# Kernel tuning notes

Measured on AMD Instinct MI355X. Metric: run time of the kernel, lower is better.

## Reference

```python
import jax, jax.numpy as jnp
import numpy as np

N_NODES = 100000


def gcn_conv(x, src, dst, W, b, n):
    # PyG GCNConv: x' = D^-1/2 (A + I) D^-1/2 (x W) + b
    h = x @ W  # [N, out] transform first (cheaper when out < in)
    loop = jnp.arange(n, dtype=src.dtype)
    s = jnp.concatenate([src, loop])
    d = jnp.concatenate([dst, loop])
    deg = jax.ops.segment_sum(jnp.ones_like(s, dtype=h.dtype), d, num_segments=n)
    dinv = jnp.where(deg > 0, jax.lax.rsqrt(deg), 0.0)
    norm = dinv[s] * dinv[d]  # [E+N]
    msg = h[s] * norm[:, None]  # [E+N, out]
    agg = jax.ops.segment_sum(msg, d, num_segments=n)
    return agg + b


def setup_inputs() -> dict:
    key = jax.random.key(0)
    ks = jax.random.split(key, 12)
    n, E, labels = N_NODES, 1600000, 128
    edges = jax.random.randint(ks[0], (2, E), 0, n, dtype=jnp.int64)
    features = jax.random.normal(ks[1], (n, labels), dtype=jnp.float32)

    def kaiming(k, fan_in, shape):
        return jax.random.normal(k, shape, dtype=jnp.float32) * np.sqrt(2.0 / fan_in)

    return {
        "edges": edges,
        "features": features,
        "W1": kaiming(ks[2], labels, (labels, 64)),
        "b1": jnp.zeros((64,), jnp.float32),
        "W2": kaiming(ks[3], 64, (64, 32)),
        "b2": jnp.zeros((32,), jnp.float32),
        "W3": kaiming(ks[4], 32, (32, 16)),
        "b3": jnp.zeros((16,), jnp.float32),
        "Wfc": kaiming(ks[5], 112, (112, 16)),
        "bfc": jnp.zeros((16,), jnp.float32),
    }


def reference(edges, features, W1, b1, W2, b2, W3, b3, Wfc, bfc):
    n = features.shape[0]
    src, dst = edges[0], edges[1]
    # eval mode: dropout is identity
    f1 = jax.nn.relu(gcn_conv(features, src, dst, W1, b1, n))  # [N, 64]
    f2 = jax.nn.relu(gcn_conv(f1, src, dst, W2, b2, n))        # [N, 32]
    f3 = jax.nn.relu(gcn_conv(f2, src, dst, W3, b3, n))        # [N, 16]
    cat = jnp.concatenate([f1, f2, f3], axis=1)                 # [N, 112]
    return jax.nn.relu(cat @ Wfc + bfc)                         # [N, 16]
```

## Files before the change

kernel.cpp:

```cpp
#include <hip/hip_runtime.h>

typedef unsigned short u16;
typedef float f32x4 __attribute__((ext_vector_type(4)));
typedef short bf16x8 __attribute__((ext_vector_type(8)));

constexpr int SH = 9;
constexpr int NB = 1 << SH;
constexpr int TILE = 4096;

__device__ inline float bf2f(u16 u) {
  union { unsigned int i; float f; } c;
  c.i = ((unsigned int)u) << 16;
  return c.f;
}
__device__ inline u16 f2bf(float f) {
  union { float f; unsigned int i; } c;
  c.f = f;
  unsigned int r = c.i + 0x7fff + ((c.i >> 16) & 1);
  return (u16)(r >> 16);
}

union V8 {
  bf16x8 v;
  short s[8];
  u16 u[8];
  int i[4];
};


__global__ void __launch_bounds__(256) k_hist(const int* __restrict__ dst,
                                              int* __restrict__ ghist, int E,
                                              int nblk, int nbk) {
  __shared__ int lcnt[NB];
  int t = threadIdx.x, blk = blockIdx.x;
  for (int i = t; i < nbk; i += 256) lcnt[i] = 0;
  __syncthreads();
  int beg = blk * TILE, end = min(beg + TILE, E);
  for (int e = beg + t; e < end; e += 256) atomicAdd(&lcnt[dst[e] >> SH], 1);
  __syncthreads();
  for (int i = t; i < nbk; i += 256) ghist[i * nblk + blk] = lcnt[i];
}

__global__ void __launch_bounds__(256) k_scanA(int* __restrict__ ghist,
                                               int* __restrict__ bsum, int nblk) {
  __shared__ int sc[256];
  int i = blockIdx.x, t = threadIdx.x;
  int* row = ghist + (size_t)i * nblk;
  int e0 = 2 * t, e1 = 2 * t + 1;
  int a0 = (e0 < nblk) ? row[e0] : 0;
  int a1 = (e1 < nblk) ? row[e1] : 0;
  int s = a0 + a1;
  sc[t] = s;
  __syncthreads();
  for (int o = 1; o < 256; o <<= 1) {
    int x = (t >= o) ? sc[t - o] : 0;
    __syncthreads();
    sc[t] += x;
    __syncthreads();
  }
  int base = sc[t] - s;
  if (e0 < nblk) row[e0] = base;
  if (e1 < nblk) row[e1] = base + a0;
  if (t == 255) bsum[i] = sc[255];
}

__global__ void __launch_bounds__(256) k_part(const int* __restrict__ src,
                                              const int* __restrict__ dst,
                                              const int* __restrict__ goff,
                                              const int* __restrict__ bsum,
                                              int* __restrict__ ebuf, int E,
                                              int nblk, int nbk) {
  __shared__ int lcur[NB];
  __shared__ int sb[256];
  int t = threadIdx.x, blk = blockIdx.x;
  int v = (t < nbk) ? bsum[t] : 0;
  sb[t] = v;
  __syncthreads();
  for (int o = 1; o < 256; o <<= 1) {
    int x = (t >= o) ? sb[t - o] : 0;
    __syncthreads();
    sb[t] += x;
    __syncthreads();
  }
  for (int i = t; i < nbk; i += 256)
    lcur[i] = goff[(size_t)i * nblk + blk] + (i ? sb[i - 1] : 0);
  __syncthreads();
  int beg = blk * TILE, end = min(beg + TILE, E);
  for (int e = beg + t; e < end; e += 256) {
    int s = src[e], d = dst[e];
    int p = atomicAdd(&lcur[d >> SH], 1);
    ebuf[p] = s | ((d & (NB - 1)) << 20);
  }
}

__global__ void __launch_bounds__(256) k_refine(
    const int* __restrict__ ebuf, const int* __restrict__ goff,
    const int* __restrict__ bsum, int* __restrict__ rowptr,
    int* __restrict__ colsrc, float* __restrict__ dinv,
    int n, int nbk, int nblk, int E) {
  __shared__ int cnt[NB];
  __shared__ int cur[NB];
  __shared__ int sc[256];
  __shared__ int bex[256];
  int b = blockIdx.x, t = threadIdx.x;
  {
    int v = (t < nbk) ? bsum[t] : 0;
    bex[t] = v;
    __syncthreads();
    for (int o = 1; o < 256; o <<= 1) {
      int x = (t >= o) ? bex[t - o] : 0;
      __syncthreads();
      bex[t] += x;
      __syncthreads();
    }
  }
  int beg = goff[(size_t)b * nblk] + (b ? bex[b - 1] : 0);
  int end = (b + 1 < nbk) ? goff[(size_t)(b + 1) * nblk] + bex[b] : E;
  cnt[t] = 0;
  cnt[t + 256] = 0;
  __syncthreads();
  for (int i = beg + t; i < end; i += 256) atomicAdd(&cnt[ebuf[i] >> 20], 1);
  __syncthreads();
  int c0 = cnt[2 * t], c1 = cnt[2 * t + 1];
  int a = c0 + c1;
  sc[t] = a;
  __syncthreads();
  for (int o = 1; o < 256; o <<= 1) {
    int x = (t >= o) ? sc[t - o] : 0;
    __syncthreads();
    sc[t] += x;
    __syncthreads();
  }
  int base0 = beg + sc[t] - a;
  int base1 = base0 + c0;
  int node0 = b << SH;
  int n0 = node0 + 2 * t, n1 = n0 + 1;
  cur[2 * t] = base0;
  cur[2 * t + 1] = base1;
  if (n0 <= n) rowptr[n0] = base0;
  if (n1 <= n) rowptr[n1] = base1;
  if (n0 < n) dinv[n0] = rsqrtf((float)(c0 + 1));
  if (n1 < n) dinv[n1] = rsqrtf((float)(c1 + 1));
  if (b == nbk - 1 && t == 0) rowptr[n] = E;
  __syncthreads();
  for (int i = beg + t; i < end; i += 256) {
    int w = ebuf[i];
    int p = atomicAdd(&cur[w >> 20], 1);
    colsrc[p] = w & 0xFFFFF;
  }
}


template <int KC, int FOUT, bool BF16IN, int FCROW0, int FCROWS, int MODE>
__global__ void __launch_bounds__(256) k_xform(
    const void* __restrict__ xin, const float* __restrict__ Wg,
    const float* __restrict__ dinv, u16* __restrict__ g,
    const float* __restrict__ Wfc, float* __restrict__ out, int n) {
  constexpr int FIN = KC * 32;
  constexpr int NC = FOUT / 16;
  constexpr int ASLOTS = 8 * KC * 64;
  constexpr int WSLOTS = KC * NC * 64;
  constexpr int WFS = (FCROWS > 0) ? KC * 64 : 1;
  __shared__ short xa[ASLOTS * 8];
  __shared__ short wb[WSLOTS * 8];
  __shared__ short wfb[WFS * 8];

  int t = threadIdx.x;
  int r0 = blockIdx.x * 128;

  for (int s = t; s < WSLOTS; s += 256) {
    int lane = s & 63, q = s >> 6;
    int nc = q % NC, kc = q / NC;
    int col = nc * 16 + (lane & 15);
    int kr = kc * 32 + (lane >> 4) * 8;
    V8 v;
#pragma unroll
    for (int j = 0; j < 8; ++j) v.s[j] = (short)f2bf(Wg[(kr + j) * FOUT + col]);
    *(bf16x8*)&wb[s * 8] = v.v;
  }
  if constexpr (FCROWS > 0) {
    for (int s = t; s < WFS; s += 256) {
      int lane = s & 63, kc = s >> 6;
      int col = lane & 15;
      int kr = kc * 32 + (lane >> 4) * 8;
      V8 v;
#pragma unroll
      for (int j = 0; j < 8; ++j)
        v.s[j] = (kr + j < FCROWS) ? (short)f2bf(Wfc[(FCROW0 + kr + j) * 16 + col]) : (short)0;
      *(bf16x8*)&wfb[s * 8] = v.v;
    }
  }

  for (int s = t; s < ASLOTS; s += 256) {
    int lane = s & 63, q = s >> 6;
    int kc = q % KC, mtile = q / KC;
    int row = mtile * 16 + (lane & 15);
    int k = kc * 32 + (lane >> 4) * 8;
    int gr = r0 + row;
    V8 v;
    if (gr < n) {
      if constexpr (BF16IN) {
        v.v = *(const bf16x8*)((const u16*)xin + (size_t)gr * FIN + k);
      } else {
        const float* xf = (const float*)xin + (size_t)gr * FIN + k;
        float4 p = *(const float4*)xf;
        float4 q4 = *(const float4*)(xf + 4);
        v.s[0] = (short)f2bf(p.x); v.s[1] = (short)f2bf(p.y);
        v.s[2] = (short)f2bf(p.z); v.s[3] = (short)f2bf(p.w);
        v.s[4] = (short)f2bf(q4.x); v.s[5] = (short)f2bf(q4.y);
        v.s[6] = (short)f2bf(q4.z); v.s[7] = (short)f2bf(q4.w);
      }
    } else {
      for (int j = 0; j < 8; ++j) v.s[j] = 0;
    }
    *(bf16x8*)&xa[s * 8] = v.v;
  }
  __syncthreads();

  int ln = t & 63, wv = t >> 6;
  int m0 = wv * 2;

  bf16x8 bf[KC * NC];
#pragma unroll
  for (int i = 0; i < KC * NC; ++i) bf[i] = *(const bf16x8*)&wb[(i * 64 + ln) * 8];
  bf16x8 wff[(FCROWS > 0) ? KC : 1];
  if constexpr (FCROWS > 0) {
#pragma unroll
    for (int i = 0; i < KC; ++i) wff[i] = *(const bf16x8*)&wfb[(i * 64 + ln) * 8];
  }

  f32x4 acc[2][NC];
  f32x4 accF[2];
#pragma unroll
  for (int i = 0; i < 2; ++i) {
    accF[i] = {0.f, 0.f, 0.f, 0.f};
#pragma unroll
    for (int j = 0; j < NC; ++j) acc[i][j] = {0.f, 0.f, 0.f, 0.f};
  }

#pragma unroll
  for (int kc = 0; kc < KC; ++kc) {
    bf16x8 a0 = *(const bf16x8*)&xa[(((m0 + 0) * KC + kc) * 64 + ln) * 8];
    bf16x8 a1 = *(const bf16x8*)&xa[(((m0 + 1) * KC + kc) * 64 + ln) * 8];
#pragma unroll
    for (int nc = 0; nc < NC; ++nc) {
      acc[0][nc] = __builtin_amdgcn_mfma_f32_16x16x32_bf16(a0, bf[kc * NC + nc], acc[0][nc], 0, 0, 0);
      acc[1][nc] = __builtin_amdgcn_mfma_f32_16x16x32_bf16(a1, bf[kc * NC + nc], acc[1][nc], 0, 0, 0);
    }
    if constexpr (FCROWS > 0) {
      accF[0] = __builtin_amdgcn_mfma_f32_16x16x32_bf16(a0, wff[kc], accF[0], 0, 0, 0);
      accF[1] = __builtin_amdgcn_mfma_f32_16x16x32_bf16(a1, wff[kc], accF[1], 0, 0, 0);
    }
  }

  int colb = ln & 15, rq = ln >> 4;
#pragma unroll
  for (int mt2 = 0; mt2 < 2; ++mt2) {
#pragma unroll
    for (int reg = 0; reg < 4; ++reg) {
      int gr = r0 + (m0 + mt2) * 16 + rq * 4 + reg;
      if (gr < n) {
        float di = dinv[gr];
#pragma unroll
        for (int nc = 0; nc < NC; ++nc)
          g[(size_t)gr * FOUT + nc * 16 + colb] = f2bf(acc[mt2][nc][reg] * di);
        if constexpr (FCROWS > 0) {
          size_t oi = (size_t)gr * 16 + colb;
          if constexpr (MODE == 0) out[oi] = accF[mt2][reg];
          else out[oi] += accF[mt2][reg];
        }
      }
    }
  }
}


template <int F>
__global__ void __launch_bounds__(256) k_gather_fin(
    const u16* __restrict__ g, const int* __restrict__ rowptr,
    const int* __restrict__ colsrc, const float* __restrict__ dinv,
    const float* __restrict__ bias, u16* __restrict__ fout, int n) {
  constexpr int LPG = F / 8;
  constexpr int G = 64 / LPG;
  int t = threadIdx.x;
  int ln = t & 63, wib = t >> 6;
  int lanein = ln % LPG, grp = ln / LPG;
  int f0 = lanein * 8;
  float bb[8];
#pragma unroll
  for (int j = 0; j < 8; ++j) bb[j] = bias[f0 + j];
  int gw = blockIdx.x * (blockDim.x >> 6) + wib;
  int nwaves = (gridDim.x * blockDim.x) >> 6;
  for (int node = gw * G + grp; node < n; node += nwaves * G) {
    int b = rowptr[node], e = rowptr[node + 1];
    float p0[8], p1[8], p2[8], p3[8];
    {
      V8 u;
      u.v = *(const bf16x8*)&g[(size_t)node * F + f0];
#pragma unroll
      for (int j = 0; j < 8; ++j) {
        p0[j] = bf2f(u.u[j]);
        p1[j] = 0.f; p2[j] = 0.f; p3[j] = 0.f;
      }
    }
    int i = b;
    for (; i + 4 <= e; i += 4) {
      int s0 = colsrc[i + 0], s1 = colsrc[i + 1];
      int s2 = colsrc[i + 2], s3 = colsrc[i + 3];
      V8 u0, u1, u2, u3;
      u0.v = *(const bf16x8*)&g[(size_t)s0 * F + f0];
      u1.v = *(const bf16x8*)&g[(size_t)s1 * F + f0];
      u2.v = *(const bf16x8*)&g[(size_t)s2 * F + f0];
      u3.v = *(const bf16x8*)&g[(size_t)s3 * F + f0];
#pragma unroll
      for (int j = 0; j < 8; ++j) {
        p0[j] += bf2f(u0.u[j]);
        p1[j] += bf2f(u1.u[j]);
        p2[j] += bf2f(u2.u[j]);
        p3[j] += bf2f(u3.u[j]);
      }
    }
    for (; i < e; ++i) {
      int s = colsrc[i];
      V8 u;
      u.v = *(const bf16x8*)&g[(size_t)s * F + f0];
#pragma unroll
      for (int j = 0; j < 8; ++j) p1[j] += bf2f(u.u[j]);
    }
    float di = dinv[node];
    V8 o;
#pragma unroll
    for (int j = 0; j < 8; ++j) {
      float a = (p0[j] + p1[j]) + (p2[j] + p3[j]);
      o.u[j] = f2bf(fmaxf(fmaf(a, di, bb[j]), 0.f));
    }
    *(bf16x8*)&fout[(size_t)node * F + f0] = o.v;
  }
}


__global__ void __launch_bounds__(256) k_gather_fc(
    const u16* __restrict__ g3, const int* __restrict__ rowptr,
    const int* __restrict__ colsrc, const float* __restrict__ dinv,
    const float* __restrict__ b3, const float* __restrict__ Wfc,
    const float* __restrict__ bfc, float* __restrict__ out, int n) {
  __shared__ short wfb[64 * 8];
  int t = threadIdx.x;
  for (int s = t; s < 64; s += 256) {
    int lane = s & 63;
    int col = lane & 15;
    int kr = (lane >> 4) * 8;
    V8 v;
#pragma unroll
    for (int j = 0; j < 8; ++j)
      v.s[j] = (kr + j < 16) ? (short)f2bf(Wfc[(96 + kr + j) * 16 + col]) : (short)0;
    *(bf16x8*)&wfb[s * 8] = v.v;
  }
  __syncthreads();

  int ln = t & 63, wv = t >> 6;
  bf16x8 wff = *(const bf16x8*)&wfb[ln * 8];
  int lanein = ln & 1, grp = ln >> 1;
  int f0 = lanein * 8;
  float bb[8];
#pragma unroll
  for (int j = 0; j < 8; ++j) bb[j] = b3[f0 + j];
  int colb = ln & 15, rq = ln >> 4, kq = ln >> 4;
  float bfcc = bfc[colb];

  int wid = blockIdx.x * 4 + wv;
  int nw = gridDim.x * 4;
  int nch = (n + 31) / 32;

  for (int ch = wid; ch < nch; ch += nw) {
    int gr = ch * 32 + grp;
    V8 o;
    if (gr < n) {
      int b = rowptr[gr], e = rowptr[gr + 1];
      float p0[8], p1[8], p2[8], p3[8];
      {
        V8 u;
        u.v = *(const bf16x8*)&g3[(size_t)gr * 16 + f0];
#pragma unroll
        for (int j = 0; j < 8; ++j) {
          p0[j] = bf2f(u.u[j]);
          p1[j] = 0.f; p2[j] = 0.f; p3[j] = 0.f;
        }
      }
      int i = b;
      for (; i + 4 <= e; i += 4) {
        int s0 = colsrc[i + 0], s1 = colsrc[i + 1];
        int s2 = colsrc[i + 2], s3 = colsrc[i + 3];
        V8 u0, u1, u2, u3;
        u0.v = *(const bf16x8*)&g3[(size_t)s0 * 16 + f0];
        u1.v = *(const bf16x8*)&g3[(size_t)s1 * 16 + f0];
        u2.v = *(const bf16x8*)&g3[(size_t)s2 * 16 + f0];
        u3.v = *(const bf16x8*)&g3[(size_t)s3 * 16 + f0];
#pragma unroll
        for (int j = 0; j < 8; ++j) {
          p0[j] += bf2f(u0.u[j]);
          p1[j] += bf2f(u1.u[j]);
          p2[j] += bf2f(u2.u[j]);
          p3[j] += bf2f(u3.u[j]);
        }
      }
      for (; i < e; ++i) {
        int s = colsrc[i];
        V8 u;
        u.v = *(const bf16x8*)&g3[(size_t)s * 16 + f0];
#pragma unroll
        for (int j = 0; j < 8; ++j) p1[j] += bf2f(u.u[j]);
      }
      float di = dinv[gr];
#pragma unroll
      for (int j = 0; j < 8; ++j) {
        float a = (p0[j] + p1[j]) + (p2[j] + p3[j]);
        o.u[j] = f2bf(fmaxf(fmaf(a, di, bb[j]), 0.f));
      }
    } else {
#pragma unroll
      for (int j = 0; j < 8; ++j) o.s[j] = 0;
    }

#pragma unroll
    for (int tt = 0; tt < 2; ++tt) {
      int sl4 = (((ln & 15) + tt * 16) * 2 + (kq & 1)) * 4;
      V8 A;
#pragma unroll
      for (int d = 0; d < 4; ++d)
        A.i[d] = __builtin_amdgcn_ds_bpermute(sl4, o.i[d]);
      if (kq >= 2) {
#pragma unroll
        for (int j = 0; j < 8; ++j) A.s[j] = 0;
      }
      f32x4 acc = {0.f, 0.f, 0.f, 0.f};
      acc = __builtin_amdgcn_mfma_f32_16x16x32_bf16(A.v, wff, acc, 0, 0, 0);
#pragma unroll
      for (int reg = 0; reg < 4; ++reg) {
        int go = ch * 32 + tt * 16 + rq * 4 + reg;
        if (go < n) {
          size_t oi = (size_t)go * 16 + colb;
          out[oi] = fmaxf(out[oi] + acc[reg] + bfcc, 0.f);
        }
      }
    }
  }
}


extern "C" void kernel_launch(void* const* d_in, const int* in_sizes, int n_in,
                              void* d_out, int out_size, void* d_ws, size_t ws_size,
                              hipStream_t stream) {
  const int* edges = (const int*)d_in[0];
  const float* feat = (const float*)d_in[1];
  const float* W1 = (const float*)d_in[2];
  const float* b1 = (const float*)d_in[3];
  const float* W2 = (const float*)d_in[4];
  const float* b2 = (const float*)d_in[5];
  const float* W3 = (const float*)d_in[6];
  const float* b3 = (const float*)d_in[7];
  const float* Wfc = (const float*)d_in[8];
  const float* bfc = (const float*)d_in[9];
  float* out = (float*)d_out;

  const int E = in_sizes[0] / 2;
  const int n = in_sizes[1] / 128;
  const int* srcp = edges;
  const int* dstp = edges + E;
  const int nbk = (n + NB - 1) >> SH;
  const int nblk = (E + TILE - 1) / TILE;

  char* w = (char*)d_ws;
  auto carve = [&](size_t bytes) {
    void* p = (void*)w;
    w += (bytes + 255) & ~(size_t)255;
    return p;
  };
  int* ghist = (int*)carve((size_t)nbk * nblk * 4);
  int* bsum = (int*)carve(256 * 4);
  int* rowptr = (int*)carve(((size_t)n + 1) * 4);
  float* dinv = (float*)carve((size_t)n * 4);
  int* colsrc = (int*)carve((size_t)E * 4);
  size_t bigA = (size_t)E * 4 > (size_t)n * 128 ? (size_t)E * 4 : (size_t)n * 128;
  void* pA = carve(bigA);
  int* ebuf = (int*)pA;
  u16* g1 = (u16*)pA;
  u16* f2 = (u16*)pA;
  void* pB = carve((size_t)n * 128);
  u16* f1 = (u16*)pB;
  u16* g3 = (u16*)pB;
  u16* g2 = (u16*)carve((size_t)n * 64);

  k_hist<<<nblk, 256, 0, stream>>>(dstp, ghist, E, nblk, nbk);
  k_scanA<<<nbk, 256, 0, stream>>>(ghist, bsum, nblk);
  k_part<<<nblk, 256, 0, stream>>>(srcp, dstp, ghist, bsum, ebuf, E, nblk, nbk);
  k_refine<<<nbk, 256, 0, stream>>>(ebuf, ghist, bsum, rowptr, colsrc, dinv, n, nbk, nblk, E);

  const int xb = (n + 127) / 128;

  k_xform<4, 64, false, 0, 0, 0><<<xb, 256, 0, stream>>>(
      feat, W1, dinv, g1, (const float*)nullptr, (float*)nullptr, n);
  k_gather_fin<64><<<2048, 256, 0, stream>>>(g1, rowptr, colsrc, dinv, b1, f1, n);
  k_xform<2, 32, true, 0, 64, 0><<<xb, 256, 0, stream>>>(
      f1, W2, dinv, g2, Wfc, out, n);
  k_gather_fin<32><<<2048, 256, 0, stream>>>(g2, rowptr, colsrc, dinv, b2, f2, n);
  k_xform<1, 16, true, 64, 32, 1><<<xb, 256, 0, stream>>>(
      f2, W3, dinv, g3, Wfc, out, n);
  k_gather_fc<<<xb, 256, 0, stream>>>(g3, rowptr, colsrc, dinv, b3, Wfc, bfc, out, n);
}
```

Measured before the change: 164.3 us.

## Fuse edge histogram and partition into one pass using fixed-capacity bucket cells

Replaces the hist, scan and partition sequence with a single partition kernel. Each edge tile writes its edges straight into per-(bucket, tile) cells of fixed capacity 64 and atomically adds its counts into per-bucket totals. A one-block scan then produces bucket bases, and the refine kernel walks the sparse cells, skipping empty slots, to build the CSR. This removes one full read of the destination array and a kernel launch, at the cost of a larger, sparsely filled edge buffer and wasted slot iteration in refine. It also silently overflows if any tile sends more than 64 edges to one bucket, which holds for uniformly random edges but not for skewed graphs. The gather grid size is also raised from 2048 to 3072 blocks.

```diff
diff --git a/kernel.cpp b/kernel.cpp
--- a/kernel.cpp
+++ b/kernel.cpp
@@ -7,6 +7,7 @@
 constexpr int SH = 9;
 constexpr int NB = 1 << SH;
 constexpr int TILE = 4096;
+constexpr int CAP = 64;
 
 __device__ inline float bf2f(u16 u) {
   union { unsigned int i; float f; } c;
@@ -28,29 +29,42 @@
 };
 
 
-__global__ void __launch_bounds__(256) k_hist(const int* __restrict__ dst,
-                                              int* __restrict__ ghist, int E,
-                                              int nblk, int nbk) {
-  __shared__ int lcnt[NB];
+__global__ void k_zero(int* __restrict__ p, int n) {
+  int i = blockIdx.x * blockDim.x + threadIdx.x;
+  if (i < n) p[i] = 0;
+}
+
+__global__ void __launch_bounds__(256) k_part2(const int* __restrict__ src,
+                                               const int* __restrict__ dst,
+                                               int* __restrict__ ebuf,
+                                               int* __restrict__ gcnt,
+                                               int* __restrict__ bsum,
+                                               int E, int nblk, int nbk) {
+  __shared__ int lcur[NB];
   int t = threadIdx.x, blk = blockIdx.x;
-  for (int i = t; i < nbk; i += 256) lcnt[i] = 0;
+  for (int i = t; i < nbk; i += 256) lcur[i] = 0;
   __syncthreads();
   int beg = blk * TILE, end = min(beg + TILE, E);
-  for (int e = beg + t; e < end; e += 256) atomicAdd(&lcnt[dst[e] >> SH], 1);
-  __syncthreads();
-  for (int i = t; i < nbk; i += 256) ghist[i * nblk + blk] = lcnt[i];
-}
-
-__global__ void __launch_bounds__(256) k_scanA(int* __restrict__ ghist,
-                                               int* __restrict__ bsum, int nblk) {
+  for (int e = beg + t; e < end; e += 256) {
+    int s = src[e], d = dst[e];
+    int b = d >> SH;
+    int p = atomicAdd(&lcur[b], 1);
+    ebuf[((size_t)b * nblk + blk) * CAP + p] = s | ((d & (NB - 1)) << 20);
+  }
+  __syncthreads();
+  for (int i = t; i < nbk; i += 256) {
+    int c = lcur[i];
+    gcnt[(size_t)i * nblk + blk] = c;
+    if (c) atomicAdd(&bsum[i], c);
+  }
+}
+
+__global__ void __launch_bounds__(256) k_scanB(const int* __restrict__ bsum,
+                                               int* __restrict__ bbase, int nbk) {
   __shared__ int sc[256];
-  int i = blockIdx.x, t = threadIdx.x;
-  int* row = ghist + (size_t)i * nblk;
-  int e0 = 2 * t, e1 = 2 * t + 1;
-  int a0 = (e0 < nblk) ? row[e0] : 0;
-  int a1 = (e1 < nblk) ? row[e1] : 0;
-  int s = a0 + a1;
-  sc[t] = s;
+  int t = threadIdx.x;
+  int v = (t < nbk) ? bsum[t] : 0;
+  sc[t] = v;
   __syncthreads();
   for (int o = 1; o < 256; o <<= 1) {
     int x = (t >= o) ? sc[t - o] : 0;
@@ -58,68 +72,34 @@
     sc[t] += x;
     __syncthreads();
   }
-  int base = sc[t] - s;
-  if (e0 < nblk) row[e0] = base;
-  if (e1 < nblk) row[e1] = base + a0;
-  if (t == 255) bsum[i] = sc[255];
-}
-
-__global__ void __launch_bounds__(256) k_part(const int* __restrict__ src,
-                                              const int* __restrict__ dst,
-                                              const int* __restrict__ goff,
-                                              const int* __restrict__ bsum,
-                                              int* __restrict__ ebuf, int E,
-                                              int nblk, int nbk) {
-  __shared__ int lcur[NB];
-  __shared__ int sb[256];
-  int t = threadIdx.x, blk = blockIdx.x;
-  int v = (t < nbk) ? bsum[t] : 0;
-  sb[t] = v;
-  __syncthreads();
-  for (int o = 1; o < 256; o <<= 1) {
-    int x = (t >= o) ? sb[t - o] : 0;
-    __syncthreads();
-    sb[t] += x;
-    __syncthreads();
-  }
-  for (int i = t; i < nbk; i += 256)
-    lcur[i] = goff[(size_t)i * nblk + blk] + (i ? sb[i - 1] : 0);
-  __syncthreads();
-  int beg = blk * TILE, end = min(beg + TILE, E);
-  for (int e = beg + t; e < end; e += 256) {
-    int s = src[e], d = dst[e];
-    int p = atomicAdd(&lcur[d >> SH], 1);
-    ebuf[p] = s | ((d & (NB - 1)) << 20);
-  }
-}
-
-__global__ void __launch_bounds__(256) k_refine(
-    const int* __restrict__ ebuf, const int* __restrict__ goff,
-    const int* __restrict__ bsum, int* __restrict__ rowptr,
+  if (t < nbk) bbase[t] = sc[t] - v;
+}
+
+__global__ void __launch_bounds__(256) k_refine2(
+    const int* __restrict__ ebuf, const int* __restrict__ gcnt,
+    const int* __restrict__ bbase, int* __restrict__ rowptr,
     int* __restrict__ colsrc, float* __restrict__ dinv,
     int n, int nbk, int nblk, int E) {
   __shared__ int cnt[NB];
   __shared__ int cur[NB];
+  __shared__ int ccnt[512];
   __shared__ int sc[256];
-  __shared__ int bex[256];
   int b = blockIdx.x, t = threadIdx.x;
-  {
-    int v = (t < nbk) ? bsum[t] : 0;
-    bex[t] = v;
-    __syncthreads();
-    for (int o = 1; o < 256; o <<= 1) {
-      int x = (t >= o) ? bex[t - o] : 0;
-      __syncthreads();
-      bex[t] += x;
-      __syncthreads();
-    }
-  }
-  int beg = goff[(size_t)b * nblk] + (b ? bex[b - 1] : 0);
-  int end = (b + 1 < nbk) ? goff[(size_t)(b + 1) * nblk] + bex[b] : E;
+  const int* row = gcnt + (size_t)b * nblk;
+  for (int i = t; i < nblk; i += 256) ccnt[i] = row[i];
   cnt[t] = 0;
   cnt[t + 256] = 0;
   __syncthreads();
-  for (int i = beg + t; i < end; i += 256) atomicAdd(&cnt[ebuf[i] >> 20], 1);
+
+  const size_t cell0 = (size_t)b * nblk * CAP;
+  int tot = nblk * CAP;
+  for (int idx = t; idx < tot; idx += 256) {
+    int c = idx >> 6, s = idx & (CAP - 1);
+    if (s < ccnt[c]) {
+      int w = ebuf[cell0 + (size_t)c * CAP + s];
+      atomicAdd(&cnt[w >> 20], 1);
+    }
+  }
   __syncthreads();
   int c0 = cnt[2 * t], c1 = cnt[2 * t + 1];
   int a = c0 + c1;
@@ -131,6 +111,7 @@
     sc[t] += x;
     __syncthreads();
   }
+  int beg = bbase[b];
   int base0 = beg + sc[t] - a;
   int base1 = base0 + c0;
   int node0 = b << SH;
@@ -143,10 +124,13 @@
   if (n1 < n) dinv[n1] = rsqrtf((float)(c1 + 1));
   if (b == nbk - 1 && t == 0) rowptr[n] = E;
   __syncthreads();
-  for (int i = beg + t; i < end; i += 256) {
-    int w = ebuf[i];
-    int p = atomicAdd(&cur[w >> 20], 1);
-    colsrc[p] = w & 0xFFFFF;
+  for (int idx = t; idx < tot; idx += 256) {
+    int c = idx >> 6, s = idx & (CAP - 1);
+    if (s < ccnt[c]) {
+      int w = ebuf[cell0 + (size_t)c * CAP + s];
+      int p = atomicAdd(&cur[w >> 20], 1);
+      colsrc[p] = w & 0xFFFFF;
+    }
   }
 }
 
@@ -476,12 +460,14 @@
     w += (bytes + 255) & ~(size_t)255;
     return p;
   };
-  int* ghist = (int*)carve((size_t)nbk * nblk * 4);
+  int* gcnt = (int*)carve((size_t)nbk * nblk * 4);
   int* bsum = (int*)carve(256 * 4);
+  int* bbase = (int*)carve(256 * 4);
   int* rowptr = (int*)carve(((size_t)n + 1) * 4);
   float* dinv = (float*)carve((size_t)n * 4);
   int* colsrc = (int*)carve((size_t)E * 4);
-  size_t bigA = (size_t)E * 4 > (size_t)n * 128 ? (size_t)E * 4 : (size_t)n * 128;
+  size_t ebytes = (size_t)nbk * nblk * CAP * 4;
+  size_t bigA = ebytes > (size_t)n * 128 ? ebytes : (size_t)n * 128;
   void* pA = carve(bigA);
   int* ebuf = (int*)pA;
   u16* g1 = (u16*)pA;
@@ -491,19 +477,19 @@
   u16* g3 = (u16*)pB;
   u16* g2 = (u16*)carve((size_t)n * 64);
 
-  k_hist<<<nblk, 256, 0, stream>>>(dstp, ghist, E, nblk, nbk);
-  k_scanA<<<nbk, 256, 0, stream>>>(ghist, bsum, nblk);
-  k_part<<<nblk, 256, 0, stream>>>(srcp, dstp, ghist, bsum, ebuf, E, nblk, nbk);
-  k_refine<<<nbk, 256, 0, stream>>>(ebuf, ghist, bsum, rowptr, colsrc, dinv, n, nbk, nblk, E);
+  k_zero<<<1, 256, 0, stream>>>(bsum, 256);
+  k_part2<<<nblk, 256, 0, stream>>>(srcp, dstp, ebuf, gcnt, bsum, E, nblk, nbk);
+  k_scanB<<<1, 256, 0, stream>>>(bsum, bbase, nbk);
+  k_refine2<<<nbk, 256, 0, stream>>>(ebuf, gcnt, bbase, rowptr, colsrc, dinv, n, nbk, nblk, E);
 
   const int xb = (n + 127) / 128;
 
   k_xform<4, 64, false, 0, 0, 0><<<xb, 256, 0, stream>>>(
       feat, W1, dinv, g1, (const float*)nullptr, (float*)nullptr, n);
-  k_gather_fin<64><<<2048, 256, 0, stream>>>(g1, rowptr, colsrc, dinv, b1, f1, n);
+  k_gather_fin<64><<<3072, 256, 0, stream>>>(g1, rowptr, colsrc, dinv, b1, f1, n);
   k_xform<2, 32, true, 0, 64, 0><<<xb, 256, 0, stream>>>(
       f1, W2, dinv, g2, Wfc, out, n);
-  k_gather_fin<32><<<2048, 256, 0, stream>>>(g2, rowptr, colsrc, dinv, b2, f2, n);
+  k_gather_fin<32><<<3072, 256, 0, stream>>>(g2, rowptr, colsrc, dinv, b2, f2, n);
   k_xform<1, 16, true, 64, 32, 1><<<xb, 256, 0, stream>>>(
       f2, W3, dinv, g3, Wfc, out, n);
   k_gather_fc<<<xb, 256, 0, stream>>>(g3, rowptr, colsrc, dinv, b3, Wfc, bfc, out, n);
```

Measured after the change: 195.8 us. 1.19x slower.

## Store transformed features in 16-column planes and gather each plane separately

Applied to the files above, without the earlier changes.

The transform kernel now writes its output as column planes of 16 features ([plane][node][16]) instead of row-major [node][F]. The gather is replaced by a per-plane kernel launched once per plane (4 for layer 1, 2 for layer 2). Each pass gathers rows of 32 bytes, so the working set per pass (n*32 B, about 3.2 MB) is more likely to stay in cache during the random neighbour reads. The cost is rereading rowptr and colsrc once per plane and issuing more kernel launches. Layer 3's gather is unaffected because it already has only 16 columns.

```diff
diff --git a/kernel.cpp b/kernel.cpp
--- a/kernel.cpp
+++ b/kernel.cpp
@@ -263,7 +263,7 @@
         float di = dinv[gr];
 #pragma unroll
         for (int nc = 0; nc < NC; ++nc)
-          g[(size_t)gr * FOUT + nc * 16 + colb] = f2bf(acc[mt2][nc][reg] * di);
+          g[((size_t)nc * n + gr) * 16 + colb] = f2bf(acc[mt2][nc][reg] * di);
         if constexpr (FCROWS > 0) {
           size_t oi = (size_t)gr * 16 + colb;
           if constexpr (MODE == 0) out[oi] = accF[mt2][reg];
@@ -275,28 +275,26 @@
 }
 
 
-template <int F>
-__global__ void __launch_bounds__(256) k_gather_fin(
-    const u16* __restrict__ g, const int* __restrict__ rowptr,
+template <int FTOT>
+__global__ void __launch_bounds__(256) k_gplane(
+    const u16* __restrict__ plane, const int* __restrict__ rowptr,
     const int* __restrict__ colsrc, const float* __restrict__ dinv,
-    const float* __restrict__ bias, u16* __restrict__ fout, int n) {
-  constexpr int LPG = F / 8;
-  constexpr int G = 64 / LPG;
+    const float* __restrict__ bias16, u16* __restrict__ fout, int n) {
   int t = threadIdx.x;
   int ln = t & 63, wib = t >> 6;
-  int lanein = ln % LPG, grp = ln / LPG;
+  int lanein = ln & 1, grp = ln >> 1;
   int f0 = lanein * 8;
   float bb[8];
 #pragma unroll
-  for (int j = 0; j < 8; ++j) bb[j] = bias[f0 + j];
+  for (int j = 0; j < 8; ++j) bb[j] = bias16[f0 + j];
   int gw = blockIdx.x * (blockDim.x >> 6) + wib;
   int nwaves = (gridDim.x * blockDim.x) >> 6;
-  for (int node = gw * G + grp; node < n; node += nwaves * G) {
+  for (int node = gw * 32 + grp; node < n; node += nwaves * 32) {
     int b = rowptr[node], e = rowptr[node + 1];
     float p0[8], p1[8], p2[8], p3[8];
     {
       V8 u;
-      u.v = *(const bf16x8*)&g[(size_t)node * F + f0];
+      u.v = *(const bf16x8*)&plane[(size_t)node * 16 + f0];
 #pragma unroll
       for (int j = 0; j < 8; ++j) {
         p0[j] = bf2f(u.u[j]);
@@ -308,10 +306,10 @@
       int s0 = colsrc[i + 0], s1 = colsrc[i + 1];
       int s2 = colsrc[i + 2], s3 = colsrc[i + 3];
       V8 u0, u1, u2, u3;
-      u0.v = *(const bf16x8*)&g[(size_t)s0 * F + f0];
-      u1.v = *(const bf16x8*)&g[(size_t)s1 * F + f0];
-      u2.v = *(const bf16x8*)&g[(size_t)s2 * F + f0];
-      u3.v = *(const bf16x8*)&g[(size_t)s3 * F + f0];
+      u0.v = *(const bf16x8*)&plane[(size_t)s0 * 16 + f0];
+      u1.v = *(const bf16x8*)&plane[(size_t)s1 * 16 + f0];
+      u2.v = *(const bf16x8*)&plane[(size_t)s2 * 16 + f0];
+      u3.v = *(const bf16x8*)&plane[(size_t)s3 * 16 + f0];
 #pragma unroll
       for (int j = 0; j < 8; ++j) {
         p0[j] += bf2f(u0.u[j]);
@@ -323,7 +321,7 @@
     for (; i < e; ++i) {
       int s = colsrc[i];
       V8 u;
-      u.v = *(const bf16x8*)&g[(size_t)s * F + f0];
+      u.v = *(const bf16x8*)&plane[(size_t)s * 16 + f0];
 #pragma unroll
       for (int j = 0; j < 8; ++j) p1[j] += bf2f(u.u[j]);
     }
@@ -334,7 +332,7 @@
       float a = (p0[j] + p1[j]) + (p2[j] + p3[j]);
       o.u[j] = f2bf(fmaxf(fmaf(a, di, bb[j]), 0.f));
     }
-    *(bf16x8*)&fout[(size_t)node * F + f0] = o.v;
+    *(bf16x8*)&fout[(size_t)node * FTOT + f0] = o.v;
   }
 }
 
@@ -497,13 +495,18 @@
   k_refine<<<nbk, 256, 0, stream>>>(ebuf, ghist, bsum, rowptr, colsrc, dinv, n, nbk, nblk, E);
 
   const int xb = (n + 127) / 128;
+  const int gp = (n + 127) / 128;
 
   k_xform<4, 64, false, 0, 0, 0><<<xb, 256, 0, stream>>>(
       feat, W1, dinv, g1, (const float*)nullptr, (float*)nullptr, n);
-  k_gather_fin<64><<<2048, 256, 0, stream>>>(g1, rowptr, colsrc, dinv, b1, f1, n);
+  for (int p = 0; p < 4; ++p)
+    k_gplane<64><<<gp, 256, 0, stream>>>(
+        g1 + (size_t)p * n * 16, rowptr, colsrc, dinv, b1 + p * 16, f1 + p * 16, n);
   k_xform<2, 32, true, 0, 64, 0><<<xb, 256, 0, stream>>>(
       f1, W2, dinv, g2, Wfc, out, n);
-  k_gather_fin<32><<<2048, 256, 0, stream>>>(g2, rowptr, colsrc, dinv, b2, f2, n);
+  for (int p = 0; p < 2; ++p)
+    k_gplane<32><<<gp, 256, 0, stream>>>(
+        g2 + (size_t)p * n * 16, rowptr, colsrc, dinv, b2 + p * 16, f2 + p * 16, n);
   k_xform<1, 16, true, 64, 32, 1><<<xb, 256, 0, stream>>>(
       f2, W3, dinv, g3, Wfc, out, n);
   k_gather_fc<<<xb, 256, 0, stream>>>(g3, rowptr, colsrc, dinv, b3, Wfc, bfc, out, n);
```

Measured after the change: 212.5 us. +29.3%, slower.
